# Optimization experiments

Hardware: AMD Instinct MI355X
Metric: run time of the kernel (lower is better)

## Reference

```python
import jax, jax.numpy as jnp
from jax import lax
import numpy as np

EPS = 1e-5
CH = [16, 64, 512]


def _conv(x, w, stride):
    # x: [B,D,H,W,Cin], w: [3,3,3,Cin,Cout], centered kernel (padding 1) like ME kernel_size=3
    return lax.conv_general_dilated(
        x, w, (stride, stride, stride), [(1, 1)] * 3,
        dimension_numbers=('NDHWC', 'DHWIO', 'NDHWC'))


def _bn_elu(x, m, gamma, beta):
    # BatchNorm over ACTIVE sites only (ME stores features only at active coords), training-mode stats.
    mm = m[..., None]
    cnt = jnp.sum(m)
    mean = jnp.sum(x * mm, axis=(0, 1, 2, 3)) / cnt
    var = jnp.sum(jnp.square(x - mean) * mm, axis=(0, 1, 2, 3)) / cnt
    xh = (x - mean) * lax.rsqrt(var + EPS) * gamma + beta
    return jax.nn.elu(xh) * mm


def _pool_mask(m):
    # ME stride-2 conv output coords = unique(in_coord // 2) -> OR over 2x2x2 blocks
    return lax.reduce_window(m, 0.0, lax.max, (1, 2, 2, 2), (1, 2, 2, 2), 'VALID')


def _block(x, m_in, wa, ga, ba, wb, gb, bb):
    m_out = _pool_mask(m_in)
    y = _conv(x, wa, 2) * m_out[..., None]   # strided sparse conv, masked to output coords
    y = _bn_elu(y, m_out, ga, ba)
    y = _conv(y, wb, 1) * m_out[..., None]   # stride-1 conv keeps coordinate set
    y = _bn_elu(y, m_out, gb, bb)
    return y, m_out


def setup_inputs() -> dict:
    key = jax.random.key(0)
    ks = jax.random.split(key, 16)
    B, G = 4, 128
    x = jax.random.normal(ks[0], (B, G, G, G, 1), dtype=jnp.float32)
    mask = jax.random.randint(ks[1], (B, G, G, G), 0, 2, dtype=jnp.int32)

    def kconv(k, cin, cout):
        std = np.sqrt(2.0 / (27 * cout))  # kaiming_normal_ fan_out, relu
        return jax.random.normal(k, (3, 3, 3, cin, cout), dtype=jnp.float32) * std

    inp = {'x': x, 'mask': mask,
           'w1a': kconv(ks[2], 1, CH[0]),  'g1a': jnp.ones((CH[0],)), 'b1a': jnp.zeros((CH[0],)),
           'w1b': kconv(ks[3], CH[0], CH[0]), 'g1b': jnp.ones((CH[0],)), 'b1b': jnp.zeros((CH[0],)),
           'w2a': kconv(ks[4], CH[0], CH[1]), 'g2a': jnp.ones((CH[1],)), 'b2a': jnp.zeros((CH[1],)),
           'w2b': kconv(ks[5], CH[1], CH[1]), 'g2b': jnp.ones((CH[1],)), 'b2b': jnp.zeros((CH[1],)),
           'w3a': kconv(ks[6], CH[1], CH[2]), 'g3a': jnp.ones((CH[2],)), 'b3a': jnp.zeros((CH[2],)),
           'w3b': kconv(ks[7], CH[2], CH[2]), 'g3b': jnp.ones((CH[2],)), 'b3b': jnp.zeros((CH[2],)),
           'wm': jax.random.normal(ks[8], (CH[2], CH[2]), dtype=jnp.float32) / np.sqrt(CH[2]),
           'bm': jnp.zeros((CH[2],)),
           'wv': jax.random.normal(ks[9], (CH[2], CH[2]), dtype=jnp.float32) / np.sqrt(CH[2]),
           'bv': jnp.zeros((CH[2],))}
    return inp


def reference(x, mask, w1a, g1a, b1a, w1b, g1b, b1b,
              w2a, g2a, b2a, w2b, g2b, b2b,
              w3a, g3a, b3a, w3b, g3b, b3b,
              wm, bm, wv, bv):
    m0 = mask.astype(jnp.float32)
    h = x * m0[..., None]  # features exist only at active coordinates
    h, m1 = _block(h, m0, w1a, g1a, b1a, w1b, g1b, b1b)
    h, m2 = _block(h, m1, w2a, g2a, b2a, w2b, g2b, b2b)
    h, m3 = _block(h, m2, w3a, g3a, b3a, w3b, g3b, b3b)
    # MinkowskiGlobalPooling: per-batch mean over active sites -> [B, 512]
    denom = jnp.sum(m3, axis=(1, 2, 3), keepdims=False)[:, None]
    pooled = jnp.sum(h * m3[..., None], axis=(1, 2, 3)) / denom
    mean = pooled @ wm + bm
    log_var = pooled @ wv + bv
    return mean, log_var
```

## Files before the change

kernel.cpp:

```cpp
#include <hip/hip_runtime.h>
#include <cstddef>


#define EPSV 1e-5f

typedef _Float16 f16x4 __attribute__((ext_vector_type(4)));
typedef _Float16 f16x8 __attribute__((ext_vector_type(8)));
typedef float f32x4 __attribute__((ext_vector_type(4)));

template <int KC> struct FragSel;
template <> struct FragSel<32> { using T = f16x8; };
template <> struct FragSel<16> { using T = f16x4; };

__device__ __forceinline__ f32x4 mfma16(f16x8 a, f16x8 b, f32x4 c) {
    return __builtin_amdgcn_mfma_f32_16x16x32_f16(a, b, c, 0, 0, 0);
}
__device__ __forceinline__ f32x4 mfma16(f16x4 a, f16x4 b, f32x4 c) {
    return __builtin_amdgcn_mfma_f32_16x16x16f16(a, b, c, 0, 0, 0);
}

__device__ __forceinline__ void gld16(const void* g, void* l) {
    __builtin_amdgcn_global_load_lds(
        (const __attribute__((address_space(1))) unsigned int*)g,
        (__attribute__((address_space(3))) unsigned int*)l, 16, 0, 0);
}

__device__ __forceinline__ int swz(int b) { return b ^ ((b >> 3) & 0x70); }

__global__ __launch_bounds__(256) void poolf_kernel(const float* __restrict__ min_,
                                                    float* __restrict__ mout,
                                                    int Nout, int lnout,
                                                    float* __restrict__ cnt_total,
                                                    float* __restrict__ cnt_batch) {
    int voxel = blockIdx.x * 256 + threadIdx.x;
    int Nin = Nout * 2;
    int wo = voxel & (Nout - 1);
    int ho = (voxel >> lnout) & (Nout - 1);
    int dd = (voxel >> (2 * lnout)) & (Nout - 1);
    int b = voxel >> (3 * lnout);
    float mx = 0.f;
#pragma unroll
    for (int dz = 0; dz < 2; ++dz)
#pragma unroll
        for (int hy = 0; hy < 2; ++hy)
#pragma unroll
            for (int wx = 0; wx < 2; ++wx) {
                size_t idx = ((size_t)((b * Nin + 2 * dd + dz) * Nin + 2 * ho + hy)) * Nin
                             + 2 * wo + wx;
                mx = fmaxf(mx, min_[idx]);
            }
    mout[voxel] = mx;
    __shared__ float red[256];
    red[threadIdx.x] = mx;
    __syncthreads();
    for (int st = 128; st > 0; st >>= 1) {
        if (threadIdx.x < st) red[threadIdx.x] += red[threadIdx.x + st];
        __syncthreads();
    }
    if (threadIdx.x == 0) {
        atomicAdd(cnt_total, red[0]);
        if (cnt_batch) atomicAdd(&cnt_batch[b], red[0]);
    }
}

__global__ __launch_bounds__(256) void wtrans_all(
    const float* __restrict__ w1b, const float* __restrict__ w2a,
    const float* __restrict__ w2b, const float* __restrict__ w3a,
    const float* __restrict__ w3b,
    _Float16* __restrict__ o1b, _Float16* __restrict__ o2a,
    _Float16* __restrict__ o2b, _Float16* __restrict__ o3a,
    _Float16* __restrict__ o3b) {
    __shared__ float tile[32][33];
    int bid = blockIdx.x;
    const float* W; _Float16* O; int CIN, COUT, rel, TCO;
    if (bid < 27)        { W = w1b; O = o1b; CIN = 16;  COUT = 16;  rel = bid;        TCO = 1; }
    else if (bid < 81)   { W = w2a; O = o2a; CIN = 16;  COUT = 64;  rel = bid - 27;   TCO = 2; }
    else if (bid < 189)  { W = w2b; O = o2b; CIN = 64;  COUT = 64;  rel = bid - 81;   TCO = 2; }
    else if (bid < 1053) { W = w3a; O = o3a; CIN = 64;  COUT = 512; rel = bid - 189;  TCO = 16; }
    else                 { W = w3b; O = o3b; CIN = 512; COUT = 512; rel = bid - 1053; TCO = 16; }
    int TCI = (CIN + 31) >> 5;
    int per_t = TCI * TCO;
    int t = rel / per_t;
    int rr = rel - t * per_t;
    int tci = rr / TCO, tco = rr - tci * TCO;
    int ci0 = tci * 32, co0 = tco * 32;
    int tid = threadIdx.x;
    int c32 = tid & 31, r8 = tid >> 5;
#pragma unroll
    for (int j = 0; j < 4; ++j) {
        int ci = ci0 + j * 8 + r8, co = co0 + c32;
        if (ci < CIN && co < COUT)
            tile[j * 8 + r8][c32] = W[((size_t)t * CIN + ci) * COUT + co];
    }
    __syncthreads();
#pragma unroll
    for (int j = 0; j < 4; ++j) {
        int co = co0 + j * 8 + r8, ci = ci0 + c32;
        if (co < COUT && ci < CIN)
            O[((size_t)t * COUT + co) * CIN + ci] = (_Float16)tile[c32][j * 8 + r8];
    }
}

__global__ __launch_bounds__(256) void conv1a_kernel(const float* __restrict__ x,
                                                     const int* __restrict__ mask,
                                                     const float* __restrict__ w,
                                                     float* __restrict__ m1,
                                                     _Float16* __restrict__ out,
                                                     float* __restrict__ stats,
                                                     float* __restrict__ cnt_total) {
    int voxel = blockIdx.x * 256 + threadIdx.x;
    int wo = voxel & 63, ho = (voxel >> 6) & 63, dd = (voxel >> 12) & 63, b = voxel >> 18;

    int any = 0;
#pragma unroll
    for (int dz = 0; dz < 2; ++dz)
#pragma unroll
        for (int hy = 0; hy < 2; ++hy)
#pragma unroll
            for (int wx = 0; wx < 2; ++wx) {
                size_t idx = ((size_t)((b * 128 + 2 * dd + dz) * 128 + 2 * ho + hy)) * 128
                             + 2 * wo + wx;
                any |= mask[idx];
            }
    float mv = any ? 1.f : 0.f;
    m1[voxel] = mv;

    float acc[16];
#pragma unroll
    for (int i = 0; i < 16; ++i) acc[i] = 0.f;
    for (int kd = 0; kd < 3; ++kd) {
        int id = 2 * dd + kd - 1;
        if ((unsigned)id >= 128u) continue;
        for (int kh = 0; kh < 3; ++kh) {
            int ih = 2 * ho + kh - 1;
            if ((unsigned)ih >= 128u) continue;
            for (int kw = 0; kw < 3; ++kw) {
                int iw = 2 * wo + kw - 1;
                if ((unsigned)iw >= 128u) continue;
                size_t idx = ((size_t)((b * 128 + id) * 128 + ih)) * 128 + iw;
                float xv = x[idx] * (float)mask[idx];
                const float* wp = w + ((kd * 3 + kh) * 3 + kw) * 16;
#pragma unroll
                for (int co = 0; co < 16; ++co) acc[co] = fmaf(xv, wp[co], acc[co]);
            }
        }
    }
    _Float16* op = out + (size_t)voxel * 16;
    __shared__ float red[256 * 32];
    __shared__ float redm[256];
#pragma unroll
    for (int co = 0; co < 16; ++co) {
        float v = acc[co] * mv;
        op[co] = (_Float16)v;
        red[threadIdx.x * 32 + co] = v;
        red[threadIdx.x * 32 + 16 + co] = v * v;
    }
    redm[threadIdx.x] = mv;
    __syncthreads();
    for (int st = 128; st > 0; st >>= 1) {
        if (threadIdx.x < st) {
#pragma unroll
            for (int k = 0; k < 32; ++k)
                red[threadIdx.x * 32 + k] += red[(threadIdx.x + st) * 32 + k];
            redm[threadIdx.x] += redm[threadIdx.x + st];
        }
        __syncthreads();
    }
    if (threadIdx.x < 32) {
        float* sb = stats + (blockIdx.x & 7) * 32;
        atomicAdd(&sb[threadIdx.x], red[threadIdx.x]);
    }
    if (threadIdx.x == 32) atomicAdd(cnt_total, redm[0]);
}

template <int CIN, int COUT, int NTILE, int STRIDE, int NIN, int NOUT,
          int TW, int LTW, int TH, int LTH, int TD, int WM, int MINW, int TAPG,
          bool STATS, bool FUSEIN>
__global__ __launch_bounds__(256, MINW) void conv_mfma(const _Float16* __restrict__ in,
                                                       const _Float16* __restrict__ wt,
                                                       const float* __restrict__ mout,
                                                       _Float16* __restrict__ out,
                                                       const _Float16* __restrict__ zbuf,
                                                       float* __restrict__ stats,
                                                       const float* __restrict__ min_,
                                                       const float* __restrict__ statsi,
                                                       const float* __restrict__ cnti,
                                                       const float* __restrict__ gin,
                                                       const float* __restrict__ bin) {
    constexpr int M = TW * TH * TD;
    constexpr int KC = (CIN >= 32) ? 32 : 16;
    constexpr int KB = KC * 2;
    constexpr int LKB = (KC >= 32) ? 6 : 5;
    constexpr int HW_ = (TW - 1) * STRIDE + 3;
    constexpr int HH_ = (TH - 1) * STRIDE + 3;
    constexpr int HD_ = (TD - 1) * STRIDE + 3;
    constexpr int HV = HW_ * HH_ * HD_;
    constexpr int LPV = KB / 16;
    constexpr int VPI = 64 / LPV;
    constexpr int NIH = (HV + VPI - 1) / VPI;
    constexpr int HVP = NIH * VPI;
    constexpr int WN = 4 / WM;
    constexpr int WMT = M / WM;
    constexpr int WNT = NTILE / WN;
    constexpr int NAF = WMT / 16;
    constexpr int NBF = WNT / 16;
    constexpr int NBLK = COUT / NTILE;
    constexpr int NTW = NOUT / TW, NTH = NOUT / TH, NTD = NOUT / TD;
    constexpr int NUMM = 4 * NTW * NTH * NTD;
    constexpr int BI = (NTILE * KB + 1023) / 1024;
    constexpr int NG = 27 / TAPG;
    constexpr int BTAP = NTILE * KB;
    static_assert(!FUSEIN || CIN == KC, "FUSEIN requires single K-chunk");

    using Frag = typename FragSel<KC>::T;

    __shared__ _Float16 halo[HVP * KC];
    __shared__ _Float16 bbuf[2 * TAPG * NTILE * KC];
    __shared__ float cfs[FUSEIN ? 2 * CIN : 2];

    int cpx = gridDim.x >> 3;
    int bid = (blockIdx.x & 7) * cpx + (blockIdx.x >> 3);

    int nblk = (NBLK > 1) ? bid / NUMM : 0;
    int mblk = (NBLK > 1) ? bid % NUMM : bid;
    int tw = mblk % NTW;
    int th = (mblk / NTW) % NTH;
    int td = (mblk / (NTW * NTH)) % NTD;
    int b = mblk / (NTW * NTH * NTD);
    int d0 = td * TD * STRIDE - 1, h0 = th * TH * STRIDE - 1, w0 = tw * TW * STRIDE - 1;

    int tid = threadIdx.x;
    int wv = tid >> 6, lane = tid & 63, m16 = lane & 15, quad = lane >> 4;
    int wm_ = wv % WM, wn_ = wv / WM;
    int qb = quad * (KB / 4);

    if constexpr (FUSEIN) {
        float cn = *cnti;
        for (int c = tid; c < CIN; c += 256) {
            float s = 0.f, q = 0.f;
#pragma unroll
            for (int k = 0; k < 8; ++k) {
                s += statsi[k * 2 * CIN + c];
                q += statsi[k * 2 * CIN + CIN + c];
            }
            float mean = s / cn;
            float var = q / cn - mean * mean;
            float sc = rsqrtf(var + EPSV) * gin[c];
            cfs[c] = sc;
            cfs[CIN + c] = bin[c] - mean * sc;
        }
    }

    int abase_b[NAF];
#pragma unroll
    for (int r = 0; r < NAF; ++r) {
        int vloc = wm_ * WMT + r * 16 + m16;
        int vw = vloc & (TW - 1), vh = (vloc >> LTW) & (TH - 1), vd = vloc >> (LTW + LTH);
        int avox = ((vd * STRIDE) * HH_ + vh * STRIDE) * HW_ + vw * STRIDE;
        abase_b[r] = avox * KB + qb;
    }
    int bofsw[NBF];
#pragma unroll
    for (int f = 0; f < NBF; ++f)
        bofsw[f] = swz((wn_ * WNT + f * 16 + m16) * KB + qb);

    int bsrc[2];
    bool bok[2];
#pragma unroll
    for (int k = 0; k < 2; ++k) {
        int i = wv + 4 * k;
        int S = i * 1024 + lane * 16;
        int Bq = swz(S);
        int row = Bq >> LKB;
        int cb = Bq & (KB - 1);
        bsrc[k] = row * CIN + (cb >> 1);
        bok[k] = (i < BI) && ((BTAP % 1024 == 0) || (row < NTILE));
    }

    f32x4 acc[NAF][NBF];
#pragma unroll
    for (int r = 0; r < NAF; ++r)
#pragma unroll
        for (int f = 0; f < NBF; ++f) acc[r][f] = (f32x4){0.f, 0.f, 0.f, 0.f};

    auto stage_halo = [&](int c0) {
        for (int i = wv; i < NIH; i += 4) {
            int S = i * 1024 + lane * 16;
            int Bq = swz(S);
            int hv = Bq >> LKB;
            int cb = Bq & (KB - 1);
            int hw = hv % HW_;
            int t2 = hv / HW_;
            int hh = t2 % HH_;
            int hd = t2 / HH_;
            int d = d0 + hd, h = h0 + hh, w = w0 + hw;
            bool ok = (hv < HV) && ((unsigned)d < (unsigned)NIN) &&
                      ((unsigned)h < (unsigned)NIN) && ((unsigned)w < (unsigned)NIN);
            if constexpr (FUSEIN) {
                f16x8 o = (f16x8){0, 0, 0, 0, 0, 0, 0, 0};
                if (ok) {
                    size_t gvox = ((size_t)(((b * NIN + d) * NIN + h) * NIN + w));
                    f16x8 xv = *(const f16x8*)(in + gvox * CIN + (cb >> 1));
                    float mv = min_[gvox];
                    int cc = cb >> 1;
#pragma unroll
                    for (int k = 0; k < 8; ++k) {
                        float xh = (float)xv[k] * cfs[cc + k] + cfs[CIN + cc + k];
                        float e = xh > 0.f ? xh : expm1f(xh);
                        o[k] = (_Float16)(e * mv);
                    }
                }
                *(f16x8*)((char*)halo + S) = o;
            } else {
                const _Float16* g =
                    ok ? in + ((size_t)(((b * NIN + d) * NIN + h) * NIN + w)) * CIN + c0
                             + (cb >> 1)
                       : zbuf;
                gld16(g, (char*)halo + i * 1024);
            }
        }
    };

    auto stage_B = [&](int tap, int jslot, int c0) {
        const _Float16* wb = wt + (size_t)tap * (COUT * CIN) + (size_t)nblk * NTILE * CIN + c0;
#pragma unroll
        for (int k = 0; k < 2; ++k) {
            if (bok[k])
                gld16(wb + bsrc[k], (char*)bbuf + (size_t)jslot * BTAP + (wv + 4 * k) * 1024);
        }
    };

    for (int c0 = 0; c0 < CIN; c0 += KC) {
        __syncthreads();
        stage_halo(c0);
#pragma unroll
        for (int j = 0; j < TAPG; ++j) stage_B(j, j, c0);

        for (int g = 0; g < NG; ++g) {
            __syncthreads();
            if (g + 1 < NG) {
                int tb2 = (g + 1) * TAPG;
                int js = ((g + 1) & 1) * TAPG;
#pragma unroll
                for (int j = 0; j < TAPG; ++j) stage_B(tb2 + j, js + j, c0);
            }
            int tb = g * TAPG;
            int kd = tb / 9, rr = tb - kd * 9, kh = rr / 3, kw = rr - kh * 3;
            int tvb = ((kd * HH_ + kh) * HW_ + kw) * KB;
            const char* bp = (const char*)bbuf + (size_t)((g & 1) * TAPG) * BTAP;
            __builtin_amdgcn_s_setprio(1);
#pragma unroll
            for (int j = 0; j < TAPG; ++j) {
                Frag a[NAF], bb[NBF];
#pragma unroll
                for (int r = 0; r < NAF; ++r)
                    a[r] = *(const Frag*)((const char*)halo + swz(abase_b[r] + tvb + j * KB));
#pragma unroll
                for (int f = 0; f < NBF; ++f)
                    bb[f] = *(const Frag*)(bp + (size_t)j * BTAP + bofsw[f]);
#pragma unroll
                for (int r = 0; r < NAF; ++r)
#pragma unroll
                    for (int f = 0; f < NBF; ++f) acc[r][f] = mfma16(a[r], bb[f], acc[r][f]);
            }
            __builtin_amdgcn_s_setprio(0);
        }
    }

    int n0 = nblk * NTILE + wn_ * WNT + m16;
    float sv[NBF], qv[NBF];
    if constexpr (STATS) {
#pragma unroll
        for (int f = 0; f < NBF; ++f) { sv[f] = 0.f; qv[f] = 0.f; }
    }
#pragma unroll
    for (int r = 0; r < NAF; ++r) {
#pragma unroll
        for (int j = 0; j < 4; ++j) {
            int vloc = wm_ * WMT + r * 16 + quad * 4 + j;
            int vw = vloc & (TW - 1), vh = (vloc >> LTW) & (TH - 1), vd = vloc >> (LTW + LTH);
            int od = td * TD + vd, oh = th * TH + vh, ow = tw * TW + vw;
            size_t gvox = ((size_t)((b * NOUT + od) * NOUT + oh)) * NOUT + ow;
            float mv = mout[gvox];
            _Float16* op = out + gvox * COUT + n0;
#pragma unroll
            for (int f = 0; f < NBF; ++f) {
                float val = acc[r][f][j] * mv;
                op[f * 16] = (_Float16)val;
                if constexpr (STATS) { sv[f] += val; qv[f] += val * val; }
            }
        }
    }
    if constexpr (STATS) {
        float* sb = stats + (blockIdx.x & 7) * (2 * COUT);
#pragma unroll
        for (int f = 0; f < NBF; ++f) {
            float s = sv[f], q = qv[f];
            s += __shfl_xor(s, 16);
            s += __shfl_xor(s, 32);
            q += __shfl_xor(q, 16);
            q += __shfl_xor(q, 32);
            if (lane < 16) {
                int c = n0 + f * 16;
                atomicAdd(&sb[c], s);
                atomicAdd(&sb[COUT + c], q);
            }
        }
    }
}

template <int C, int LOGC>
__global__ __launch_bounds__(256) void bn_apply2(_Float16* __restrict__ x,
                                                 const float* __restrict__ m,
                                                 const float* __restrict__ stats,
                                                 const float* __restrict__ cntp,
                                                 const float* __restrict__ gamma,
                                                 const float* __restrict__ beta, long n) {
    __shared__ float cf[2 * C];
    float cn = *cntp;
    for (int c = threadIdx.x; c < C; c += 256) {
        float s = 0.f, q = 0.f;
#pragma unroll
        for (int k = 0; k < 8; ++k) {
            s += stats[k * 2 * C + c];
            q += stats[k * 2 * C + C + c];
        }
        float mean = s / cn;
        float var = q / cn - mean * mean;
        float sc = rsqrtf(var + EPSV) * gamma[c];
        cf[c] = sc;
        cf[C + c] = beta[c] - mean * sc;
    }
    __syncthreads();
    long stride = (long)gridDim.x * 2048;
    for (long i8 = ((long)blockIdx.x * 256 + threadIdx.x) * 8; i8 < n; i8 += stride) {
        int c = (int)(i8 & (C - 1));
        long v = i8 >> LOGC;
        f16x8 xv = *(const f16x8*)(x + i8);
        float mv = m[v];
        f16x8 o;
#pragma unroll
        for (int k = 0; k < 8; ++k) {
            float xh = (float)xv[k] * cf[c + k] + cf[C + c + k];
            float e = xh > 0.f ? xh : expm1f(xh);
            o[k] = (_Float16)(e * mv);
        }
        *(f16x8*)(x + i8) = o;
    }
}

__global__ __launch_bounds__(256) void gpool_kernel(const _Float16* __restrict__ h,
                                                    const float* __restrict__ m3,
                                                    const float* __restrict__ stats,
                                                    const float* __restrict__ cntp,
                                                    const float* __restrict__ gamma,
                                                    const float* __restrict__ beta,
                                                    float* __restrict__ pooled) {
    __shared__ float cf[1024];
    float cn = *cntp;
    for (int c = threadIdx.x; c < 512; c += 256) {
        float s = 0.f, q = 0.f;
#pragma unroll
        for (int k = 0; k < 8; ++k) {
            s += stats[k * 1024 + c];
            q += stats[k * 1024 + 512 + c];
        }
        float mean = s / cn;
        float var = q / cn - mean * mean;
        float sc = rsqrtf(var + EPSV) * gamma[c];
        cf[c] = sc;
        cf[512 + c] = beta[c] - mean * sc;
    }
    __syncthreads();
    int b = blockIdx.x >> 6, seg = blockIdx.x & 63;
    int ch = (threadIdx.x & 63) * 8;
    int v0 = threadIdx.x >> 6;
    float scl[8], shf[8];
#pragma unroll
    for (int k = 0; k < 8; ++k) {
        scl[k] = cf[ch + k];
        shf[k] = cf[512 + ch + k];
    }
    float s[8];
#pragma unroll
    for (int k = 0; k < 8; ++k) s[k] = 0.f;
    for (int v = v0; v < 64; v += 4) {
        int vox = b * 4096 + seg * 64 + v;
        float mv = m3[vox];
        f16x8 xv = *(const f16x8*)(h + (size_t)vox * 512 + ch);
#pragma unroll
        for (int k = 0; k < 8; ++k) {
            float xh = (float)xv[k] * scl[k] + shf[k];
            float e = xh > 0.f ? xh : expm1f(xh);
            s[k] += e * mv;
        }
    }
#pragma unroll
    for (int k = 0; k < 8; ++k) atomicAdd(&pooled[b * 512 + ch + k], s[k]);
}

__global__ __launch_bounds__(256) void head_kernel(const float* __restrict__ pooled,
                                                   const float* __restrict__ cntb,
                                                   const float* __restrict__ wm,
                                                   const float* __restrict__ bm,
                                                   const float* __restrict__ wv,
                                                   const float* __restrict__ bv,
                                                   float* __restrict__ out) {
    int t = blockIdx.x * 256 + threadIdx.x;
    int which = t >> 11;
    int b = (t >> 9) & 3;
    int j = t & 511;
    const float* W = which ? wv : wm;
    float bias = which ? bv[j] : bm[j];
    const float* p = pooled + b * 512;
    float s = 0.f;
    for (int c = 0; c < 512; ++c) s = fmaf(p[c], W[c * 512 + j], s);
    out[t] = s / cntb[b] + bias;
}

extern "C" void kernel_launch(void* const* d_in, const int* in_sizes, int n_in,
                              void* d_out, int out_size, void* d_ws, size_t ws_size,
                              hipStream_t stream) {
    const float* x   = (const float*)d_in[0];
    const int* mask  = (const int*)d_in[1];
    const float* w1a = (const float*)d_in[2];
    const float* g1a = (const float*)d_in[3];
    const float* b1a = (const float*)d_in[4];
    const float* w1b = (const float*)d_in[5];
    const float* g1b = (const float*)d_in[6];
    const float* b1b = (const float*)d_in[7];
    const float* w2a = (const float*)d_in[8];
    const float* g2a = (const float*)d_in[9];
    const float* b2a = (const float*)d_in[10];
    const float* w2b = (const float*)d_in[11];
    const float* g2b = (const float*)d_in[12];
    const float* b2b = (const float*)d_in[13];
    const float* w3a = (const float*)d_in[14];
    const float* g3a = (const float*)d_in[15];
    const float* b3a = (const float*)d_in[16];
    const float* w3b = (const float*)d_in[17];
    const float* g3b = (const float*)d_in[18];
    const float* b3b = (const float*)d_in[19];
    const float* wm  = (const float*)d_in[20];
    const float* bm  = (const float*)d_in[21];
    const float* wv  = (const float*)d_in[22];
    const float* bv  = (const float*)d_in[23];
    float* out = (float*)d_out;

    char* ws = (char*)d_ws;
    _Float16* A  = (_Float16*)(ws + 0);
    _Float16* Bb = (_Float16*)(ws + 33554432);
    _Float16* w1bh = (_Float16*)(ws + 67108864);
    _Float16* w2ah = (_Float16*)(ws + 67125248);
    _Float16* w2bh = (_Float16*)(ws + 67182592);
    _Float16* w3ah = (_Float16*)(ws + 67403776);
    _Float16* w3bh = (_Float16*)(ws + 69173248);
    float* m1 = (float*)(ws + 83329024);
    float* m2 = (float*)(ws + 87523328);
    float* m3 = (float*)(ws + 88047616);
    float* counts = (float*)(ws + 88113152);
    float* stats  = (float*)(ws + 88113216);
    float* pooled = (float*)(ws + 88309824);
    _Float16* zbuf = (_Float16*)(ws + 88318016);

    float* sL0 = stats;
    float* sL1 = stats + 1 * 8192;
    float* sL2 = stats + 2 * 8192;
    float* sL3 = stats + 3 * 8192;
    float* sL4 = stats + 4 * 8192;
    float* sL5 = stats + 5 * 8192;

    _Float16* h1a = A;
    _Float16* h1b = Bb;
    _Float16* h2a = A;
    _Float16* h2b = Bb;
    _Float16* h3a = A;
    _Float16* h3b = Bb;

    hipMemsetAsync(counts, 0, 64 + 196608 + 8192 + 256, stream);

    wtrans_all<<<7965, 256, 0, stream>>>(w1b, w2a, w2b, w3a, w3b,
                                         w1bh, w2ah, w2bh, w3ah, w3bh);

    conv1a_kernel<<<4096, 256, 0, stream>>>(x, mask, w1a, m1, h1a, sL0, counts + 0);
    poolf_kernel<<<512, 256, 0, stream>>>(m1, m2, 32, 5, counts + 1, nullptr);
    poolf_kernel<<<64, 256, 0, stream>>>(m2, m3, 16, 4, counts + 2, counts + 4);

    conv_mfma<16, 16, 16, 1, 64, 64, 8, 3, 8, 3, 8, 4, 4, 3, true, true>
        <<<2048, 256, 0, stream>>>(h1a, w1bh, m1, h1b, zbuf, sL1,
                                   m1, sL0, counts + 0, g1a, b1a);

    conv_mfma<16, 64, 64, 2, 64, 32, 8, 3, 4, 2, 4, 2, 2, 3, true, true>
        <<<1024, 256, 0, stream>>>(h1b, w2ah, m2, h2a, zbuf, sL2,
                                   m1, sL1, counts + 0, g1b, b1b);
    bn_apply2<64, 6><<<1024, 256, 0, stream>>>(h2a, m2, sL2, counts + 1, g2a, b2a, 8388608L);

    conv_mfma<64, 64, 64, 1, 32, 32, 8, 3, 8, 3, 4, 2, 2, 3, true, false>
        <<<512, 256, 0, stream>>>(h2a, w2bh, m2, h2b, zbuf, sL3,
                                  nullptr, nullptr, nullptr, nullptr, nullptr);
    bn_apply2<64, 6><<<1024, 256, 0, stream>>>(h2b, m2, sL3, counts + 1, g2b, b2b, 8388608L);

    conv_mfma<64, 512, 128, 2, 32, 16, 4, 2, 4, 2, 4, 2, 2, 1, true, false>
        <<<1024, 256, 0, stream>>>(h2b, w3ah, m3, h3a, zbuf, sL4,
                                   nullptr, nullptr, nullptr, nullptr, nullptr);
    bn_apply2<512, 9><<<512, 256, 0, stream>>>(h3a, m3, sL4, counts + 2, g3a, b3a, 8388608L);

    conv_mfma<512, 512, 128, 1, 16, 16, 8, 3, 4, 2, 4, 2, 2, 3, true, false>
        <<<512, 256, 0, stream>>>(h3a, w3bh, m3, h3b, zbuf, sL5,
                                  nullptr, nullptr, nullptr, nullptr, nullptr);

    gpool_kernel<<<256, 256, 0, stream>>>(h3b, m3, sL5, counts + 2, g3b, b3b, pooled);
    head_kernel<<<16, 256, 0, stream>>>(pooled, counts + 4, wm, bm, wv, bv, out);
}
```

Baseline: 827.1 us.

## Fuse two mask-pool kernels and use split-barrier vmcnt waits in conv pipeline

Replaces the two pooling launches with one kernel that computes both the stride-2 and stride-4 masks and their counts from a tiled block, removing a launch and a reread of the intermediate mask. In the MFMA conv loop, the single __syncthreads per tap group is replaced by raw s_barrier plus explicit s_waitcnt vmcnt. The wait lets each wave keep the next group's weight prefetch in flight while waiting only for the current loads. This relies on exact counts of outstanding global loads per wave, so a miscount could cause a race.

```diff
diff --git a/kernel.cpp b/kernel.cpp
--- a/kernel.cpp
+++ b/kernel.cpp
@@ -27,17 +27,17 @@
 
 __device__ __forceinline__ int swz(int b) { return b ^ ((b >> 3) & 0x70); }
 
-__global__ __launch_bounds__(256) void poolf_kernel(const float* __restrict__ min_,
-                                                    float* __restrict__ mout,
-                                                    int Nout, int lnout,
-                                                    float* __restrict__ cnt_total,
-                                                    float* __restrict__ cnt_batch) {
-    int voxel = blockIdx.x * 256 + threadIdx.x;
-    int Nin = Nout * 2;
-    int wo = voxel & (Nout - 1);
-    int ho = (voxel >> lnout) & (Nout - 1);
-    int dd = (voxel >> (2 * lnout)) & (Nout - 1);
-    int b = voxel >> (3 * lnout);
+__global__ __launch_bounds__(256) void pool23_kernel(const float* __restrict__ m1,
+                                                     float* __restrict__ m2,
+                                                     float* __restrict__ m3,
+                                                     float* __restrict__ cnt2,
+                                                     float* __restrict__ cnt3,
+                                                     float* __restrict__ cnt3b) {
+    int bid = blockIdx.x;
+    int tw4 = bid & 3, th4 = (bid >> 2) & 3, td8 = (bid >> 4) & 7, b = bid >> 7;
+    int tid = threadIdx.x;
+    int lw = tid & 7, lh = (tid >> 3) & 7, ld = tid >> 6;
+    int wo = tw4 * 8 + lw, ho = th4 * 8 + lh, dd = td8 * 4 + ld;
     float mx = 0.f;
 #pragma unroll
     for (int dz = 0; dz < 2; ++dz)
@@ -45,21 +45,44 @@
         for (int hy = 0; hy < 2; ++hy)
 #pragma unroll
             for (int wx = 0; wx < 2; ++wx) {
-                size_t idx = ((size_t)((b * Nin + 2 * dd + dz) * Nin + 2 * ho + hy)) * Nin
+                size_t idx = ((size_t)((b * 64 + 2 * dd + dz) * 64 + 2 * ho + hy)) * 64
                              + 2 * wo + wx;
-                mx = fmaxf(mx, min_[idx]);
-            }
-    mout[voxel] = mx;
+                mx = fmaxf(mx, m1[idx]);
+            }
+    m2[((size_t)((b * 32 + dd) * 32 + ho)) * 32 + wo] = mx;
+
     __shared__ float red[256];
-    red[threadIdx.x] = mx;
+    __shared__ float red3[32];
+    red[tid] = mx;
+    __syncthreads();
+    if (((tid & 1) | ((tid >> 3) & 1) | ((tid >> 6) & 1)) == 0) {
+        float v = red[tid];
+        v = fmaxf(v, red[tid ^ 1]);
+        v = fmaxf(v, red[tid ^ 8]);
+        v = fmaxf(v, red[tid ^ 9]);
+        v = fmaxf(v, red[tid ^ 64]);
+        v = fmaxf(v, red[tid ^ 65]);
+        v = fmaxf(v, red[tid ^ 72]);
+        v = fmaxf(v, red[tid ^ 73]);
+        int w3 = wo >> 1, h3 = ho >> 1, d3 = dd >> 1;
+        m3[((size_t)((b * 16 + d3) * 16 + h3)) * 16 + w3] = v;
+        int i32 = (lw >> 1) + 4 * (lh >> 1) + 16 * (ld >> 1);
+        red3[i32] = v;
+    }
     __syncthreads();
     for (int st = 128; st > 0; st >>= 1) {
-        if (threadIdx.x < st) red[threadIdx.x] += red[threadIdx.x + st];
+        if (tid < st) red[tid] += red[tid + st];
         __syncthreads();
     }
-    if (threadIdx.x == 0) {
-        atomicAdd(cnt_total, red[0]);
-        if (cnt_batch) atomicAdd(&cnt_batch[b], red[0]);
+    if (tid < 16) red3[tid] += red3[tid + 16];
+    __syncthreads();
+    if (tid < 8) red3[tid] += red3[tid + 8];
+    __syncthreads();
+    if (tid == 0) {
+        float s3 = red3[0] + red3[1] + red3[2] + red3[3] + red3[4] + red3[5] + red3[6] + red3[7];
+        atomicAdd(cnt2, red[0]);
+        atomicAdd(cnt3, s3);
+        atomicAdd(&cnt3b[b], s3);
     }
 }
 
@@ -234,6 +257,8 @@
     int wm_ = wv % WM, wn_ = wv / WM;
     int qb = quad * (KB / 4);
 
+    const int nissue = ((wv < BI) ? 1 : 0) + ((wv + 4 < BI) ? 1 : 0);
+
     if constexpr (FUSEIN) {
         float cn = *cnti;
         for (int c = tid; c < CIN; c += 256) {
@@ -333,17 +358,28 @@
     for (int c0 = 0; c0 < CIN; c0 += KC) {
         __syncthreads();
         stage_halo(c0);
+        if constexpr (FUSEIN) asm volatile("s_waitcnt lgkmcnt(0)" ::: "memory");
 #pragma unroll
         for (int j = 0; j < TAPG; ++j) stage_B(j, j, c0);
 
         for (int g = 0; g < NG; ++g) {
-            __syncthreads();
+            asm volatile("s_barrier" ::: "memory");
             if (g + 1 < NG) {
                 int tb2 = (g + 1) * TAPG;
                 int js = ((g + 1) & 1) * TAPG;
 #pragma unroll
                 for (int j = 0; j < TAPG; ++j) stage_B(tb2 + j, js + j, c0);
-            }
+                if (nissue == 2)
+                    asm volatile("s_waitcnt vmcnt(%0)" :: "i"(2 * TAPG) : "memory");
+                else if (nissue == 1)
+                    asm volatile("s_waitcnt vmcnt(%0)" :: "i"(TAPG) : "memory");
+                else
+                    asm volatile("s_waitcnt vmcnt(0)" ::: "memory");
+            } else {
+                asm volatile("s_waitcnt vmcnt(0)" ::: "memory");
+            }
+            asm volatile("s_barrier" ::: "memory");
+
             int tb = g * TAPG;
             int kd = tb / 9, rr = tb - kd * 9, kh = rr / 3, kw = rr - kh * 3;
             int tvb = ((kd * HH_ + kh) * HW_ + kw) * KB;
@@ -583,8 +619,7 @@
                                          w1bh, w2ah, w2bh, w3ah, w3bh);
 
     conv1a_kernel<<<4096, 256, 0, stream>>>(x, mask, w1a, m1, h1a, sL0, counts + 0);
-    poolf_kernel<<<512, 256, 0, stream>>>(m1, m2, 32, 5, counts + 1, nullptr);
-    poolf_kernel<<<64, 256, 0, stream>>>(m2, m3, 16, 4, counts + 2, counts + 4);
+    pool23_kernel<<<512, 256, 0, stream>>>(m1, m2, m3, counts + 1, counts + 2, counts + 4);
 
     conv_mfma<16, 16, 16, 1, 64, 64, 8, 3, 8, 3, 8, 4, 4, 3, true, true>
         <<<2048, 256, 0, stream>>>(h1a, w1bh, m1, h1b, zbuf, sL1,
```

After: 840.2 us. No clear change (+1.6%).
